# Kernel tuning notes

Measured on AMD Instinct MI355X. Metric: run time of the kernel, lower is better.

Reference implementation:

```python
import jax, jax.numpy as jnp
import numpy as np

DIM = 4096
N_HEADS = 32
HEAD_DIM = 128
N_KV_HEADS = 8
KV_REPEATS = N_HEADS // N_KV_HEADS
SLIDING_WINDOW = 4096
SEQLEN = 2048
ROPE_THETA = 10000.0


def calculate_rope(x, cos_freq, sin_freq):
    # x: (S, H, D); cos/sin: (S, D//2). Rotates interleaved pairs (Mistral RoPE).
    S, H, D = x.shape
    xr = x.reshape(S, H, D // 2, 2)
    x1, x2 = xr[..., 0], xr[..., 1]
    c = cos_freq[:, None, :]
    s = sin_freq[:, None, :]
    o1 = x1 * c - x2 * s
    o2 = x1 * s + x2 * c
    return jnp.stack([o1, o2], axis=-1).reshape(S, H, D)


def setup_inputs() -> dict:
    key = jax.random.key(0)
    k0, k1, k2 = jax.random.split(key, 3)
    x = jax.random.normal(k0, (SEQLEN, DIM), dtype=jnp.float32)
    positions = jnp.arange(SEQLEN, dtype=jnp.int32)
    # RoPE frequencies
    inv_freq = 1.0 / (ROPE_THETA ** (np.arange(0, HEAD_DIM, 2, dtype=np.float32) / HEAD_DIM))
    angles = np.arange(SEQLEN, dtype=np.float32)[:, None] * inv_freq[None, :]
    cos_freq = jnp.asarray(np.cos(angles), dtype=jnp.float32)
    sin_freq = jnp.asarray(np.sin(angles), dtype=jnp.float32)
    # additive causal + sliding-window mask: 0 where allowed, -1e9 where masked
    i = np.arange(SEQLEN)
    allowed = (i[None, :] <= i[:, None]) & ((i[:, None] - i[None, :]) < SLIDING_WINDOW)
    mask = jnp.asarray(np.where(allowed, 0.0, -1e9), dtype=jnp.float32)
    cache_k = jnp.zeros((SLIDING_WINDOW, N_KV_HEADS, HEAD_DIM), dtype=jnp.float32)
    cache_v = jnp.zeros((SLIDING_WINDOW, N_KV_HEADS, HEAD_DIM), dtype=jnp.float32)
    total_head_dim = (N_HEADS + 2 * N_KV_HEADS) * HEAD_DIM
    Wqkv = jax.random.normal(k1, (total_head_dim, DIM), dtype=jnp.float32) * 0.02
    Wo = jax.random.normal(k2, (DIM, N_HEADS * HEAD_DIM), dtype=jnp.float32) * 0.02
    return {"x": x, "cos_freq": cos_freq, "sin_freq": sin_freq, "positions": positions,
            "mask": mask, "cache_k": cache_k, "cache_v": cache_v, "Wqkv": Wqkv, "Wo": Wo}


def reference(x, cos_freq, sin_freq, positions, mask, cache_k, cache_v, Wqkv, Wo):
    # Prefill branch (positions.shape[0] > 1) of Attention.__call__
    seqlen = x.shape[0]
    scale = HEAD_DIM ** (-0.5)
    s1 = N_HEADS * HEAD_DIM
    s2 = s1 + N_KV_HEADS * HEAD_DIM
    xqkv = x @ Wqkv.T                                  # (S, 6144)
    xq, xk, xv = jnp.split(xqkv, [s1, s2], axis=-1)
    xq = xq.reshape(seqlen, N_HEADS, HEAD_DIM)
    xk = xk.reshape(seqlen, N_KV_HEADS, HEAD_DIM)
    xv = xv.reshape(seqlen, N_KV_HEADS, HEAD_DIM)
    xq = calculate_rope(xq, cos_freq, sin_freq)
    xk = calculate_rope(xk, cos_freq, sin_freq)
    # KV-cache update (scatter; positions all in range here)
    cache_k = cache_k.at[positions, :, :].set(xk[positions, :, :], mode="drop")
    cache_v = cache_v.at[positions, :, :].set(xv[positions, :, :], mode="drop")
    # GQA repeat: (S, n_kv, D) -> (S, n_heads, D)
    k = jnp.repeat(xk, KV_REPEATS, axis=1)
    v = jnp.repeat(xv, KV_REPEATS, axis=1)
    q = jnp.transpose(xq, (1, 0, 2))                   # (H, S, D)
    k = jnp.transpose(k, (1, 0, 2))
    v = jnp.transpose(v, (1, 0, 2))
    scores = jnp.einsum("hqd,hkd->hqk", q, k) * scale  # (H, S, S)
    scores = scores + mask[jnp.newaxis, ...]
    probs = jax.nn.softmax(scores.astype(jnp.float32), axis=-1).astype(q.dtype)
    out = jnp.einsum("hqk,hkd->hqd", probs, v)         # (H, S, D)
    out = jnp.transpose(out, (1, 0, 2)).reshape(seqlen, -1)
    output = out @ Wo.T                                # (S, dim)
    return (output, cache_k, cache_v)
```

## Files before the change

### kernel.cpp

```cpp
#include <hip/hip_runtime.h>
#include <stdint.h>

typedef __bf16   bf16x8 __attribute__((ext_vector_type(8)));
typedef float    f32x4  __attribute__((ext_vector_type(4)));
typedef uint16_t u16x8  __attribute__((ext_vector_type(8)));

__device__ __forceinline__ uint16_t f2bf(float f) {
  uint32_t b = __builtin_bit_cast(uint32_t, f);
  b += 0x7fffu + ((b >> 16) & 1u);
  return (uint16_t)(b >> 16);
}
__device__ __forceinline__ float bf2f(uint16_t u) {
  return __builtin_bit_cast(float, ((uint32_t)u) << 16);
}
__device__ __forceinline__ u16x8 ldcvt8(const float* __restrict__ p) {
  f32x4 lo = *(const f32x4*)p;
  f32x4 hi = *(const f32x4*)(p + 4);
  u16x8 o;
  o[0] = f2bf(lo[0]); o[1] = f2bf(lo[1]); o[2] = f2bf(lo[2]); o[3] = f2bf(lo[3]);
  o[4] = f2bf(hi[0]); o[5] = f2bf(hi[1]); o[6] = f2bf(hi[2]); o[7] = f2bf(hi[3]);
  return o;
}

typedef const __attribute__((address_space(1))) uint32_t cga_u32;
typedef __attribute__((address_space(3))) uint32_t lds_u32;
__device__ __forceinline__ void gload16(const uint16_t* g, uint16_t* l) {
  __builtin_amdgcn_global_load_lds((cga_u32*)g, (lds_u32*)l, 16, 0, 0);
}

__global__ __launch_bounds__(256) void cast_kernel(const float* __restrict__ in,
                                                   uint16_t* __restrict__ out, int n8) {
  int i = blockIdx.x * 256 + threadIdx.x;
  if (i >= n8) return;
  u16x8 o = ldcvt8(in + (size_t)i * 8);
  *(u16x8*)(out + (size_t)i * 8) = o;
}

__global__ __launch_bounds__(256) void copy2_kernel(const float* __restrict__ a, float* __restrict__ da,
                                                    const float* __restrict__ b, float* __restrict__ db,
                                                    int n4) {
  int i = blockIdx.x * 256 + threadIdx.x;
  if (i >= n4) return;
  *(f32x4*)(da + (size_t)i * 4) = *(const f32x4*)(a + (size_t)i * 4);
  *(f32x4*)(db + (size_t)i * 4) = *(const f32x4*)(b + (size_t)i * 4);
}

template <int OUT_BF16>
__global__ __launch_bounds__(256) void gemm_nt_bf16(const uint16_t* __restrict__ A,
                                                    const uint16_t* __restrict__ B,
                                                    void* __restrict__ Cout,
                                                    int M, int N, int K) {
  __shared__ __align__(16) uint16_t As[128 * 32];
  __shared__ __align__(16) uint16_t Bs[128 * 32];
  const int tid = threadIdx.x;
  const int lane = tid & 63, wave = tid >> 6;
  const int l16 = lane & 15, quad = lane >> 4;
  const int wm = (wave & 1) << 6, wn = (wave >> 1) << 6;
  const int bm = blockIdx.y, bn = blockIdx.x;

  f32x4 acc[4][4] = {};

  const int srow = wave * 16 + (lane >> 2);
  const int schunk = lane & 3;
  const uint16_t* Ag = A + (size_t)(bm * 128 + srow) * K + schunk * 8;
  const uint16_t* Bg = B + (size_t)(bn * 128 + srow) * K + schunk * 8;
  const size_t rs64 = (size_t)64 * K;
  uint16_t* AsD0 = &As[srow * 32 + schunk * 8];
  uint16_t* AsD1 = AsD0 + 64 * 32;
  uint16_t* BsD0 = &Bs[srow * 32 + schunk * 8];
  uint16_t* BsD1 = BsD0 + 64 * 32;

  for (int k0 = 0; k0 < K; k0 += 32) {
    gload16(Ag, AsD0);
    gload16(Ag + rs64, AsD1);
    gload16(Bg, BsD0);
    gload16(Bg + rs64, BsD1);
    Ag += 32; Bg += 32;
    __syncthreads();
    bf16x8 af[4], bfr[4];
#pragma unroll
    for (int i = 0; i < 4; i++) {
      af[i]  = __builtin_bit_cast(bf16x8, *(const u16x8*)&As[(wm + i * 16 + l16) * 32 + quad * 8]);
      bfr[i] = __builtin_bit_cast(bf16x8, *(const u16x8*)&Bs[(wn + i * 16 + l16) * 32 + quad * 8]);
    }
#pragma unroll
    for (int i = 0; i < 4; i++)
#pragma unroll
      for (int j = 0; j < 4; j++)
        acc[i][j] = __builtin_amdgcn_mfma_f32_16x16x32_bf16(af[i], bfr[j], acc[i][j], 0, 0, 0);
    __syncthreads();
  }

  const int row0 = bm * 128 + wm + quad * 4;
  const int col0 = bn * 128 + wn + l16;
#pragma unroll
  for (int i = 0; i < 4; i++)
#pragma unroll
    for (int j = 0; j < 4; j++)
#pragma unroll
      for (int r = 0; r < 4; r++) {
        size_t idx = (size_t)(row0 + i * 16 + r) * N + (col0 + j * 16);
        if constexpr (OUT_BF16) ((uint16_t*)Cout)[idx] = f2bf(acc[i][j][r]);
        else                    ((float*)Cout)[idx]    = acc[i][j][r];
      }
}

template <int A_BF16, int OUT_BF16>
__global__ __launch_bounds__(256) void gemm_bt(const void* __restrict__ Ap,
                                               const float* __restrict__ B,
                                               void* __restrict__ Cout, int M, int N, int K) {
  constexpr int PAD = 40;
  __shared__ __align__(16) uint16_t As[128 * PAD];
  __shared__ __align__(16) uint16_t Bs[128 * PAD];
  const int tid = threadIdx.x;
  const int lane = tid & 63, wave = tid >> 6;
  const int l16 = lane & 15, quad = lane >> 4;
  const int wm = (wave & 1) << 6, wn = (wave >> 1) << 6;
  const int bm = blockIdx.y, bn = blockIdx.x;

  f32x4 acc[4][4] = {};

  const int srow = tid >> 2;
  const int scol = (tid & 3) << 3;
  const size_t aoff = (size_t)(bm * 128 + srow) * K + scol;
  const uint16_t* Agh = (const uint16_t*)Ap + aoff;
  const float*    Agf = (const float*)Ap + aoff;
  const float*    Bg  = B + (size_t)(bn * 128 + srow) * K + scol;
  const size_t rstride = (size_t)64 * K;

  for (int k0 = 0; k0 < K; k0 += 32) {
    u16x8 a0, a1;
    if constexpr (A_BF16) {
      a0 = *(const u16x8*)Agh;
      a1 = *(const u16x8*)(Agh + rstride);
      Agh += 32;
    } else {
      a0 = ldcvt8(Agf);
      a1 = ldcvt8(Agf + rstride);
      Agf += 32;
    }
    u16x8 b0 = ldcvt8(Bg);
    u16x8 b1 = ldcvt8(Bg + rstride);
    Bg += 32;
    __syncthreads();
    *(u16x8*)&As[srow * PAD + scol] = a0;
    *(u16x8*)&As[(srow + 64) * PAD + scol] = a1;
    *(u16x8*)&Bs[srow * PAD + scol] = b0;
    *(u16x8*)&Bs[(srow + 64) * PAD + scol] = b1;
    __syncthreads();
    bf16x8 af[4], bfr[4];
#pragma unroll
    for (int i = 0; i < 4; i++) {
      af[i]  = __builtin_bit_cast(bf16x8, *(const u16x8*)&As[(wm + i * 16 + l16) * PAD + quad * 8]);
      bfr[i] = __builtin_bit_cast(bf16x8, *(const u16x8*)&Bs[(wn + i * 16 + l16) * PAD + quad * 8]);
    }
#pragma unroll
    for (int i = 0; i < 4; i++)
#pragma unroll
      for (int j = 0; j < 4; j++)
        acc[i][j] = __builtin_amdgcn_mfma_f32_16x16x32_bf16(af[i], bfr[j], acc[i][j], 0, 0, 0);
  }

  const int row0 = bm * 128 + wm + quad * 4;
  const int col0 = bn * 128 + wn + l16;
#pragma unroll
  for (int i = 0; i < 4; i++)
#pragma unroll
    for (int j = 0; j < 4; j++)
#pragma unroll
      for (int r = 0; r < 4; r++) {
        size_t idx = (size_t)(row0 + i * 16 + r) * N + (col0 + j * 16);
        if constexpr (OUT_BF16) ((uint16_t*)Cout)[idx] = f2bf(acc[i][j][r]);
        else                    ((float*)Cout)[idx]    = acc[i][j][r];
      }
}

__global__ __launch_bounds__(256) void rope_kernel(const uint16_t* __restrict__ xqkv,
    const float* __restrict__ cosf, const float* __restrict__ sinf,
    const int* __restrict__ pos,
    uint16_t* __restrict__ qb, uint16_t* __restrict__ kb, uint16_t* __restrict__ vb,
    float* __restrict__ ck, float* __restrict__ cv) {
  const int s = blockIdx.x;
  const int e0 = (blockIdx.y * 256 + threadIdx.x) * 8;
  const int head = e0 >> 7;
  const int d0 = e0 & 127;
  u16x8 u = *(const u16x8*)(xqkv + (size_t)s * 6144 + e0);
  float x[8];
#pragma unroll
  for (int j = 0; j < 8; j++) x[j] = bf2f(u[j]);

  if (head < 40) {
    const int i0 = d0 >> 1;
    f32x4 c4 = *(const f32x4*)(cosf + (size_t)s * 64 + i0);
    f32x4 s4 = *(const f32x4*)(sinf + (size_t)s * 64 + i0);
    float o[8];
#pragma unroll
    for (int kk = 0; kk < 4; kk++) {
      float x1 = x[2 * kk], x2 = x[2 * kk + 1];
      o[2 * kk]     = x1 * c4[kk] - x2 * s4[kk];
      o[2 * kk + 1] = x1 * s4[kk] + x2 * c4[kk];
    }
    u16x8 ob;
#pragma unroll
    for (int j = 0; j < 8; j++) ob[j] = f2bf(o[j]);
    if (head < 32) {
      *(u16x8*)(qb + (size_t)s * 4096 + head * 128 + d0) = ob;
    } else {
      int kvh = head - 32;
      *(u16x8*)(kb + ((size_t)kvh * 2048 + s) * 128 + d0) = ob;
      int p = pos[s];
      if ((unsigned)p < 4096u) {
        float* dst = ck + ((size_t)p * 8 + kvh) * 128 + d0;
#pragma unroll
        for (int j = 0; j < 8; j++) dst[j] = o[j];
      }
    }
  } else {
    int kvh = head - 40;
    *(u16x8*)(vb + ((size_t)kvh * 2048 + s) * 128 + d0) = u;
    int p = pos[s];
    if ((unsigned)p < 4096u) {
      float* dst = cv + ((size_t)p * 8 + kvh) * 128 + d0;
#pragma unroll
      for (int j = 0; j < 8; j++) dst[j] = x[j];
    }
  }
}

__global__ __launch_bounds__(256) void vtrans_kernel(const uint16_t* __restrict__ vb,
                                                     uint16_t* __restrict__ vt) {
  __shared__ __align__(16) uint16_t t[32 * 72];
  const int h = blockIdx.z;
  const int s0 = blockIdx.x * 64, d0 = blockIdx.y * 32;
  const uint16_t* in = vb + (size_t)h * 2048 * 128;
  uint16_t* out = vt + (size_t)h * 128 * 2048;
  const int tid = threadIdx.x;
  {
    int r = tid >> 2, c8 = (tid & 3) * 8;
    u16x8 v = *(const u16x8*)(in + (size_t)(s0 + r) * 128 + d0 + c8);
#pragma unroll
    for (int j = 0; j < 8; j++) t[(c8 + j) * 72 + r] = v[j];
  }
  __syncthreads();
  {
    int r = tid >> 3, c8 = (tid & 7) * 8;
    u16x8 v = *(const u16x8*)&t[r * 72 + c8];
    *(u16x8*)(out + (size_t)(d0 + r) * 2048 + s0 + c8) = v;
  }
}

__global__ __launch_bounds__(256) void flash_kernel(const uint16_t* __restrict__ Qb,
    const uint16_t* __restrict__ Kb, const uint16_t* __restrict__ Vtb,
    uint16_t* __restrict__ Ob) {
  constexpr int QP = 136, KP = 136, VP = 72, PP = 72;
  __shared__ __align__(16) uint16_t Qs[64 * QP];
  __shared__ __align__(16) uint16_t Ks[64 * KP];
  __shared__ __align__(16) uint16_t Vts[128 * VP];
  __shared__ __align__(16) uint16_t Ps[4][16 * PP];
  const int tid = threadIdx.x;
  const int lane = tid & 63, wave = tid >> 6;
  const int l16 = lane & 15, quad = lane >> 4;
  const int qb = blockIdx.x * 64;
  const int h = blockIdx.y, kvh = h >> 2;
  const uint16_t* Qg = Qb + (size_t)qb * 4096 + h * 128;
  const uint16_t* Kg = Kb + (size_t)kvh * 2048 * 128;
  const uint16_t* Vg = Vtb + (size_t)kvh * 128 * 2048;

#pragma unroll
  for (int i = 0; i < 4; i++) {
    int c = tid + i * 256;
    int r = c >> 4, c8 = (c & 15) * 8;
    *(u16x8*)&Qs[r * QP + c8] = *(const u16x8*)(Qg + (size_t)r * 4096 + c8);
  }
  __syncthreads();
  bf16x8 qf[4];
#pragma unroll
  for (int dc = 0; dc < 4; dc++)
    qf[dc] = __builtin_bit_cast(bf16x8, *(const u16x8*)&Qs[(wave * 16 + l16) * QP + dc * 32 + quad * 8]);

  f32x4 oacc[8] = {};
  float m_run[4], l_run[4];
#pragma unroll
  for (int r = 0; r < 4; r++) { m_run[r] = -1e30f; l_run[r] = 0.f; }
  const float scale = 0.08838834764831845f;
  const int nch = blockIdx.x + 1;

  for (int ch = 0; ch < nch; ch++) {
    const int cb = ch * 64;
    __syncthreads();
#pragma unroll
    for (int i = 0; i < 4; i++) {
      int c = tid + i * 256;
      int r = c >> 4, c8 = (c & 15) * 8;
      *(u16x8*)&Ks[r * KP + c8] = *(const u16x8*)(Kg + (size_t)(cb + r) * 128 + c8);
    }
#pragma unroll
    for (int i = 0; i < 4; i++) {
      int c = tid + i * 256;
      int r = c >> 3, c8 = (c & 7) * 8;
      *(u16x8*)&Vts[r * VP + c8] = *(const u16x8*)(Vg + (size_t)r * 2048 + cb + c8);
    }
    __syncthreads();

    f32x4 sacc[4] = {};
#pragma unroll
    for (int ni = 0; ni < 4; ni++)
#pragma unroll
      for (int dc = 0; dc < 4; dc++) {
        bf16x8 kf = __builtin_bit_cast(bf16x8,
            *(const u16x8*)&Ks[(ni * 16 + l16) * KP + dc * 32 + quad * 8]);
        sacc[ni] = __builtin_amdgcn_mfma_f32_16x16x32_bf16(qf[dc], kf, sacc[ni], 0, 0, 0);
      }

    float p[4][4], alpha[4];
#pragma unroll
    for (int reg = 0; reg < 4; reg++) {
      const int q = qb + wave * 16 + quad * 4 + reg;
      float mx = -1e30f;
#pragma unroll
      for (int ni = 0; ni < 4; ni++) {
        float sv = sacc[ni][reg] * scale;
        if (cb + ni * 16 + l16 > q) sv = -1e30f;
        p[ni][reg] = sv;
        mx = fmaxf(mx, sv);
      }
#pragma unroll
      for (int off = 8; off >= 1; off >>= 1)
        mx = fmaxf(mx, __shfl_xor(mx, off, 64));
      float mn = fmaxf(m_run[reg], mx);
      alpha[reg] = __expf(m_run[reg] - mn);
      m_run[reg] = mn;
      float rs = 0.f;
#pragma unroll
      for (int ni = 0; ni < 4; ni++) {
        float e = __expf(p[ni][reg] - mn);
        p[ni][reg] = e;
        rs += e;
      }
#pragma unroll
      for (int off = 8; off >= 1; off >>= 1)
        rs += __shfl_xor(rs, off, 64);
      l_run[reg] = l_run[reg] * alpha[reg] + rs;
    }

#pragma unroll
    for (int dt = 0; dt < 8; dt++)
#pragma unroll
      for (int reg = 0; reg < 4; reg++)
        oacc[dt][reg] *= alpha[reg];

    uint16_t* Pw = Ps[wave];
#pragma unroll
    for (int ni = 0; ni < 4; ni++)
#pragma unroll
      for (int reg = 0; reg < 4; reg++)
        Pw[(quad * 4 + reg) * PP + ni * 16 + l16] = f2bf(p[ni][reg]);

    bf16x8 pf[2];
#pragma unroll
    for (int kc = 0; kc < 2; kc++)
      pf[kc] = __builtin_bit_cast(bf16x8, *(const u16x8*)&Pw[l16 * PP + kc * 32 + quad * 8]);

#pragma unroll
    for (int dt = 0; dt < 8; dt++)
#pragma unroll
      for (int kc = 0; kc < 2; kc++) {
        bf16x8 vf = __builtin_bit_cast(bf16x8,
            *(const u16x8*)&Vts[(dt * 16 + l16) * VP + kc * 32 + quad * 8]);
        oacc[dt] = __builtin_amdgcn_mfma_f32_16x16x32_bf16(pf[kc], vf, oacc[dt], 0, 0, 0);
      }
  }

#pragma unroll
  for (int dt = 0; dt < 8; dt++)
#pragma unroll
    for (int reg = 0; reg < 4; reg++) {
      float o = oacc[dt][reg] / l_run[reg];
      int row = qb + wave * 16 + quad * 4 + reg;
      int col = h * 128 + dt * 16 + l16;
      Ob[(size_t)row * 4096 + col] = f2bf(o);
    }
}

extern "C" void kernel_launch(void* const* d_in, const int* in_sizes, int n_in,
                              void* d_out, int out_size, void* d_ws, size_t ws_size,
                              hipStream_t stream) {
  const float* x     = (const float*)d_in[0];
  const float* cosf  = (const float*)d_in[1];
  const float* sinf  = (const float*)d_in[2];
  const int*   pos   = (const int*)d_in[3];
  const float* ck_in = (const float*)d_in[5];
  const float* cv_in = (const float*)d_in[6];
  const float* Wqkv  = (const float*)d_in[7];
  const float* Wo    = (const float*)d_in[8];

  float* out    = (float*)d_out;
  float* ck_out = out + (size_t)2048 * 4096;
  float* cv_out = ck_out + (size_t)4096 * 8 * 128;

  char* ws = (char*)d_ws;

  if (ws_size >= 104857600ull) {
    uint16_t* xqkv_bf = (uint16_t*)(ws);
    uint16_t* attn_bf = (uint16_t*)(ws);
    uint16_t* x_bf    = (uint16_t*)(ws + 25165824);
    uint16_t* q_bf    = (uint16_t*)(ws + 25165824);
    uint16_t* k_bf    = (uint16_t*)(ws + 41943040);
    uint16_t* v_bf    = (uint16_t*)(ws + 46137344);
    uint16_t* vt_bf   = (uint16_t*)(ws + 50331648);
    uint16_t* wq_bf   = (uint16_t*)(ws + 54525952);
    uint16_t* wo_bf   = (uint16_t*)(ws + 54525952);

    cast_kernel<<<4096, 256, 0, stream>>>(x, x_bf, 1048576);
    cast_kernel<<<12288, 256, 0, stream>>>(Wqkv, wq_bf, 3145728);

    gemm_nt_bf16<1><<<dim3(48, 16), 256, 0, stream>>>(x_bf, wq_bf, xqkv_bf, 2048, 6144, 4096);

    copy2_kernel<<<4096, 256, 0, stream>>>(ck_in, ck_out, cv_in, cv_out, 1048576);

    rope_kernel<<<dim3(2048, 3), 256, 0, stream>>>(xqkv_bf, cosf, sinf, pos,
                                                   q_bf, k_bf, v_bf, ck_out, cv_out);

    vtrans_kernel<<<dim3(32, 4, 8), 256, 0, stream>>>(v_bf, vt_bf);

    flash_kernel<<<dim3(32, 32), 256, 0, stream>>>(q_bf, k_bf, vt_bf, attn_bf);

    cast_kernel<<<8192, 256, 0, stream>>>(Wo, wo_bf, 2097152);

    gemm_nt_bf16<0><<<dim3(32, 16), 256, 0, stream>>>(attn_bf, wo_bf, out, 2048, 4096, 4096);
  } else {
    uint16_t* xqkv_bf = (uint16_t*)(ws);
    uint16_t* attn_bf = (uint16_t*)(ws);
    uint16_t* q_bf    = (uint16_t*)(ws + 25165824);
    uint16_t* k_bf    = (uint16_t*)(ws + 41943040);
    uint16_t* v_bf    = (uint16_t*)(ws + 46137344);
    uint16_t* vt_bf   = (uint16_t*)(ws + 50331648);

    gemm_bt<0, 1><<<dim3(48, 16), 256, 0, stream>>>(x, Wqkv, xqkv_bf, 2048, 6144, 4096);
    copy2_kernel<<<4096, 256, 0, stream>>>(ck_in, ck_out, cv_in, cv_out, 1048576);
    rope_kernel<<<dim3(2048, 3), 256, 0, stream>>>(xqkv_bf, cosf, sinf, pos,
                                                   q_bf, k_bf, v_bf, ck_out, cv_out);
    vtrans_kernel<<<dim3(32, 4, 8), 256, 0, stream>>>(v_bf, vt_bf);
    flash_kernel<<<dim3(32, 32), 256, 0, stream>>>(q_bf, k_bf, vt_bf, attn_bf);
    gemm_bt<1, 0><<<dim3(32, 16), 256, 0, stream>>>(attn_bf, Wo, out, 2048, 4096, 4096);
  }
}
```

Baseline: 702.2 us.

## Prefetch K/V into registers, swizzle LDS, skip masked MFMA tiles, reverse tile order

Restructures the flash attention kernel. The next K/V chunk is prefetched into registers while the current one is computed, and the padded LDS layouts are replaced by XOR-swizzled ones to avoid bank conflicts and save LDS. Q is loaded straight into registers instead of going through LDS, fully masked 16-wide MFMA sub-tiles on the diagonal are skipped, and query tiles are launched heaviest-first to balance the causal workload. Wave priority hints are also added around the MFMA blocks. The cost is more register pressure from the prefetch buffers and extra swizzle address arithmetic.

New measurement: 702.4 us. No clear change (+0.0%).

```diff
diff --git a/kernel.cpp b/kernel.cpp
--- a/kernel.cpp
+++ b/kernel.cpp
@@ -252,65 +252,84 @@
 __global__ __launch_bounds__(256) void flash_kernel(const uint16_t* __restrict__ Qb,
     const uint16_t* __restrict__ Kb, const uint16_t* __restrict__ Vtb,
     uint16_t* __restrict__ Ob) {
-  constexpr int QP = 136, KP = 136, VP = 72, PP = 72;
-  __shared__ __align__(16) uint16_t Qs[64 * QP];
-  __shared__ __align__(16) uint16_t Ks[64 * KP];
-  __shared__ __align__(16) uint16_t Vts[128 * VP];
-  __shared__ __align__(16) uint16_t Ps[4][16 * PP];
+  __shared__ __align__(16) uint16_t Ks[64 * 128];
+  __shared__ __align__(16) uint16_t Vts[128 * 64];
+  __shared__ __align__(16) uint16_t Ps[4][16 * 64];
   const int tid = threadIdx.x;
   const int lane = tid & 63, wave = tid >> 6;
   const int l16 = lane & 15, quad = lane >> 4;
-  const int qb = blockIdx.x * 64;
+  const int qtile = 31 - blockIdx.x;
+  const int qb = qtile * 64;
   const int h = blockIdx.y, kvh = h >> 2;
-  const uint16_t* Qg = Qb + (size_t)qb * 4096 + h * 128;
   const uint16_t* Kg = Kb + (size_t)kvh * 2048 * 128;
   const uint16_t* Vg = Vtb + (size_t)kvh * 128 * 2048;
 
-#pragma unroll
-  for (int i = 0; i < 4; i++) {
-    int c = tid + i * 256;
-    int r = c >> 4, c8 = (c & 15) * 8;
-    *(u16x8*)&Qs[r * QP + c8] = *(const u16x8*)(Qg + (size_t)r * 4096 + c8);
-  }
-  __syncthreads();
   bf16x8 qf[4];
-#pragma unroll
-  for (int dc = 0; dc < 4; dc++)
-    qf[dc] = __builtin_bit_cast(bf16x8, *(const u16x8*)&Qs[(wave * 16 + l16) * QP + dc * 32 + quad * 8]);
+  {
+    const uint16_t* Qg = Qb + (size_t)(qb + wave * 16 + l16) * 4096 + h * 128 + quad * 8;
+#pragma unroll
+    for (int dc = 0; dc < 4; dc++)
+      qf[dc] = __builtin_bit_cast(bf16x8, *(const u16x8*)(Qg + dc * 32));
+  }
+
+  u16x8 kreg[4], vreg[4];
+  const int krr = tid >> 4, kcb = (tid & 15) * 16;
+  const int vrr = tid >> 3, vcb = (tid & 7) * 16;
 
   f32x4 oacc[8] = {};
   float m_run[4], l_run[4];
 #pragma unroll
   for (int r = 0; r < 4; r++) { m_run[r] = -1e30f; l_run[r] = 0.f; }
   const float scale = 0.08838834764831845f;
-  const int nch = blockIdx.x + 1;
+  const int nch = qtile + 1;
+  const int qmax = qb + wave * 16 + 15;
+
+#pragma unroll
+  for (int i = 0; i < 4; i++)
+    kreg[i] = *(const u16x8*)(Kg + (size_t)(krr + i * 16) * 128 + kcb / 2);
+#pragma unroll
+  for (int i = 0; i < 4; i++)
+    vreg[i] = *(const u16x8*)(Vg + (size_t)(vrr + i * 32) * 2048 + vcb / 2);
 
   for (int ch = 0; ch < nch; ch++) {
     const int cb = ch * 64;
-    __syncthreads();
 #pragma unroll
     for (int i = 0; i < 4; i++) {
-      int c = tid + i * 256;
-      int r = c >> 4, c8 = (c & 15) * 8;
-      *(u16x8*)&Ks[r * KP + c8] = *(const u16x8*)(Kg + (size_t)(cb + r) * 128 + c8);
+      int r = krr + i * 16;
+      *(u16x8*)((char*)Ks + r * 256 + (kcb ^ ((r & 7) << 4))) = kreg[i];
     }
 #pragma unroll
     for (int i = 0; i < 4; i++) {
-      int c = tid + i * 256;
-      int r = c >> 3, c8 = (c & 7) * 8;
-      *(u16x8*)&Vts[r * VP + c8] = *(const u16x8*)(Vg + (size_t)r * 2048 + cb + c8);
-    }
-    __syncthreads();
+      int r = vrr + i * 32;
+      *(u16x8*)((char*)Vts + r * 128 + (vcb ^ ((r & 7) << 4))) = vreg[i];
+    }
+    __syncthreads();
+
+    if (ch + 1 < nch) {
+      const int nb = cb + 64;
+#pragma unroll
+      for (int i = 0; i < 4; i++)
+        kreg[i] = *(const u16x8*)(Kg + (size_t)(nb + krr + i * 16) * 128 + kcb / 2);
+#pragma unroll
+      for (int i = 0; i < 4; i++)
+        vreg[i] = *(const u16x8*)(Vg + (size_t)(vrr + i * 32) * 2048 + nb + vcb / 2);
+    }
 
     f32x4 sacc[4] = {};
-#pragma unroll
-    for (int ni = 0; ni < 4; ni++)
-#pragma unroll
-      for (int dc = 0; dc < 4; dc++) {
-        bf16x8 kf = __builtin_bit_cast(bf16x8,
-            *(const u16x8*)&Ks[(ni * 16 + l16) * KP + dc * 32 + quad * 8]);
-        sacc[ni] = __builtin_amdgcn_mfma_f32_16x16x32_bf16(qf[dc], kf, sacc[ni], 0, 0, 0);
-      }
+    __builtin_amdgcn_s_setprio(1);
+#pragma unroll
+    for (int ni = 0; ni < 4; ni++) {
+      if (cb + ni * 16 <= qmax) {
+#pragma unroll
+        for (int dc = 0; dc < 4; dc++) {
+          int r = ni * 16 + l16;
+          bf16x8 kf = __builtin_bit_cast(bf16x8,
+              *(const u16x8*)((const char*)Ks + r * 256 + ((dc * 64 + quad * 16) ^ ((r & 7) << 4))));
+          sacc[ni] = __builtin_amdgcn_mfma_f32_16x16x32_bf16(qf[dc], kf, sacc[ni], 0, 0, 0);
+        }
+      }
+    }
+    __builtin_amdgcn_s_setprio(0);
 
     float p[4][4], alpha[4];
 #pragma unroll
@@ -353,22 +372,30 @@
 #pragma unroll
     for (int ni = 0; ni < 4; ni++)
 #pragma unroll
-      for (int reg = 0; reg < 4; reg++)
-        Pw[(quad * 4 + reg) * PP + ni * 16 + l16] = f2bf(p[ni][reg]);
-
-    bf16x8 pf[2];
-#pragma unroll
-    for (int kc = 0; kc < 2; kc++)
-      pf[kc] = __builtin_bit_cast(bf16x8, *(const u16x8*)&Pw[l16 * PP + kc * 32 + quad * 8]);
-
-#pragma unroll
-    for (int dt = 0; dt < 8; dt++)
-#pragma unroll
-      for (int kc = 0; kc < 2; kc++) {
-        bf16x8 vf = __builtin_bit_cast(bf16x8,
-            *(const u16x8*)&Vts[(dt * 16 + l16) * VP + kc * 32 + quad * 8]);
-        oacc[dt] = __builtin_amdgcn_mfma_f32_16x16x32_bf16(pf[kc], vf, oacc[dt], 0, 0, 0);
-      }
+      for (int reg = 0; reg < 4; reg++) {
+        int r = quad * 4 + reg;
+        *(uint16_t*)((char*)Pw + r * 128 + ((ni * 32 + l16 * 2) ^ ((r & 7) << 4))) =
+            f2bf(p[ni][reg]);
+      }
+
+    __builtin_amdgcn_s_setprio(1);
+#pragma unroll
+    for (int kc = 0; kc < 2; kc++) {
+      if (cb + kc * 32 <= qmax) {
+        bf16x8 pf = __builtin_bit_cast(bf16x8,
+            *(const u16x8*)((const char*)Pw + l16 * 128 + ((kc * 64 + quad * 16) ^ ((l16 & 7) << 4))));
+#pragma unroll
+        for (int dt = 0; dt < 8; dt++) {
+          int r = dt * 16 + l16;
+          bf16x8 vf = __builtin_bit_cast(bf16x8,
+              *(const u16x8*)((const char*)Vts + r * 128 + ((kc * 64 + quad * 16) ^ ((r & 7) << 4))));
+          oacc[dt] = __builtin_amdgcn_mfma_f32_16x16x32_bf16(pf, vf, oacc[dt], 0, 0, 0);
+        }
+      }
+    }
+    __builtin_amdgcn_s_setprio(0);
+
+    __syncthreads();
   }
 
 #pragma unroll
```
